# Optimization experiments

Measured on AMD Instinct MI355X. Metric: run time of the kernel, lower is better.

Reference implementation:

```python
import jax, jax.numpy as jnp
import numpy as np
import math

IN_FEATURES = 512
RFF_FEATURES = 2048
OUT_FEATURES = 1000
N = 8192
RIDGE_PENALTY = 1.0
MEAN_FIELD_FACTOR = 25.0
RFF_SCALAR = math.sqrt(RFF_FEATURES / 2)  # 32.0


def _random_ortho(key, n, m):
    q, _ = jnp.linalg.qr(jax.random.normal(key, (n, m), dtype=jnp.float32))
    return q


def setup_inputs() -> dict:
    key = jax.random.key(0)
    k_d, k_w, k_norm, k_b, k_lw, k_lb, k_cov = jax.random.split(key, 7)
    D = jax.random.normal(k_d, (N, IN_FEATURES), dtype=jnp.float32)
    # RFF weight: concat of random orthonormal blocks (rff_features > in_features)
    ws = []
    dim_left = RFF_FEATURES
    kk = k_w
    while dim_left > IN_FEATURES:
        kk, sub = jax.random.split(kk)
        ws.append(_random_ortho(sub, IN_FEATURES, IN_FEATURES))
        dim_left -= IN_FEATURES
    kk, sub = jax.random.split(kk)
    ws.append(_random_ortho(sub, IN_FEATURES, dim_left))
    W = jnp.concatenate(ws, axis=1)  # [in, rff]
    feature_norm = jax.random.normal(k_norm, W.shape, dtype=jnp.float32) ** 2
    W = W * jnp.sqrt(feature_norm.sum(0))
    b = jax.random.uniform(k_b, (RFF_FEATURES,), dtype=jnp.float32) * (2.0 * math.pi)
    # logit head (nn.Linear): weight [out, rff], bias [out]
    bound = 1.0 / math.sqrt(RFF_FEATURES)
    logit_w = jax.random.uniform(k_lw, (OUT_FEATURES, RFF_FEATURES), dtype=jnp.float32,
                                 minval=-bound, maxval=bound)
    logit_b = jax.random.uniform(k_lb, (OUT_FEATURES,), dtype=jnp.float32,
                                 minval=-bound, maxval=bound)
    # positive-definite covariance buffer (stand-in for inverted precision)
    A = jax.random.normal(k_cov, (RFF_FEATURES, RFF_FEATURES), dtype=jnp.float32) * 0.01
    covariance = A @ A.T + jnp.eye(RFF_FEATURES, dtype=jnp.float32)
    return {"D": D, "W": W, "b": b, "logit_w": logit_w, "logit_b": logit_b,
            "covariance": covariance}


def reference(D, W, b, logit_w, logit_b, covariance):
    # RFF feature map: cos(D @ W + b) / rff_scalar  -> [N, rff]
    Phi = jnp.cos(D @ W + b) / RFF_SCALAR
    # linear head -> [N, out]
    pred = Phi @ logit_w.T + logit_b
    # diag(Phi @ cov @ Phi.T) * ridge computed row-wise in O(N*r^2)
    diag_cov = jnp.sum((Phi @ covariance) * Phi, axis=-1) * RIDGE_PENALTY  # [N]
    logits_scale = jnp.sqrt(1.0 + diag_cov * MEAN_FIELD_FACTOR)
    return pred / logits_scale[:, None]
```

## Files before the change

kernel.cpp:

```cpp
#include <hip/hip_runtime.h>
#include <hip/hip_fp8.h>
#include <math.h>

#define N_ROWS 8192
#define IN_F   512
#define RFF    2048
#define OUT_F  1000
#define OUT_PAD 1024
#define INV_RFF_SCALAR 0.03125f
#define MEAN_FIELD 25.0f
#define PHI_NT 24

typedef __attribute__((ext_vector_type(8))) short short8;
typedef __attribute__((ext_vector_type(4))) float f32x4;
typedef __attribute__((ext_vector_type(2))) long long2v;

__device__ __forceinline__ unsigned short f32_to_bf16(float f) {
    unsigned u = __float_as_uint(f);
    unsigned r = 0x7FFFu + ((u >> 16) & 1u);
    return (unsigned short)((u + r) >> 16);
}
__device__ __forceinline__ float bf16_to_f32(unsigned short h) {
    return __uint_as_float(((unsigned)h) << 16);
}
__device__ __forceinline__ unsigned char f32_to_fp8(float x) {
    __hip_fp8_e4m3 q(x);
    return (unsigned char)q.__x;
}

__device__ __forceinline__ int perm64(int k) {
    return (k & ~63) | (((k >> 3) & 3) << 4) | (((k >> 5) & 1) << 3) | (k & 7);
}

__device__ __forceinline__ void stage_tile64(const unsigned short* __restrict__ X,
                                             int r0, int k0, unsigned char* lds,
                                             int w, int lane) {
    #pragma unroll
    for (int h = 0; h < 4; ++h) {
        int qb = h * 256 + w * 64;
        int q = qb + lane;
        int rt = q >> 7, c = (q >> 4) & 7, r = q & 15;
        const void* g = X + (size_t)(r0 + rt * 16 + r) * RFF + k0 + c * 8;
        __builtin_amdgcn_global_load_lds(
            (const __attribute__((address_space(1))) void*)g,
            (__attribute__((address_space(3))) void*)(lds + qb * 16),
            16, 0, 0);
    }
}

__device__ __forceinline__ void stage_tile8(const unsigned char* __restrict__ X,
                                            int r0, int k0b, unsigned char* lds,
                                            int w, int lane) {
    #pragma unroll
    for (int h = 0; h < 4; ++h) {
        int qb = h * 256 + w * 64;
        int q = qb + lane;
        int rt = q >> 7, c = (q >> 4) & 7, r = q & 15;
        const void* g = X + (size_t)(r0 + rt * 16 + r) * RFF + k0b + c * 16;
        __builtin_amdgcn_global_load_lds(
            (const __attribute__((address_space(1))) void*)g,
            (__attribute__((address_space(3))) void*)(lds + qb * 16),
            16, 0, 0);
    }
}

__global__ __launch_bounds__(256) void conv_split_kernel(
    const float* __restrict__ X, unsigned short* __restrict__ H,
    unsigned short* __restrict__ L, int n4)
{
    int i = blockIdx.x * 256 + threadIdx.x;
    if (i >= n4) return;
    float4 v = ((const float4*)X)[i];
    ushort4 h, l;
    h.x = f32_to_bf16(v.x); l.x = f32_to_bf16(v.x - bf16_to_f32(h.x));
    h.y = f32_to_bf16(v.y); l.y = f32_to_bf16(v.y - bf16_to_f32(h.y));
    h.z = f32_to_bf16(v.z); l.z = f32_to_bf16(v.z - bf16_to_f32(h.z));
    h.w = f32_to_bf16(v.w); l.w = f32_to_bf16(v.w - bf16_to_f32(h.w));
    ((ushort4*)H)[i] = h;
    ((ushort4*)L)[i] = l;
}

__global__ __launch_bounds__(256) void conv_covu8_kernel(
    const float* __restrict__ X, unsigned char* __restrict__ O)
{
    int i = blockIdx.x * 256 + threadIdx.x;
    int base = i * 4;
    int row = base >> 11;
    int col = base & 2047;
    int bn = row >> 7, bk = col >> 7;
    float w = (bk < bn) ? 16.0f : (bk == bn ? 8.0f : 0.0f);
    float4 v = ((const float4*)X)[i];
    float w0 = (col + 0 == row) ? 0.0f : w;
    float w1 = (col + 1 == row) ? 0.0f : w;
    float w2 = (col + 2 == row) ? 0.0f : w;
    float w3 = (col + 3 == row) ? 0.0f : w;
    uchar4 o;
    o.x = f32_to_fp8(v.x * w0); o.y = f32_to_fp8(v.y * w1);
    o.z = f32_to_fp8(v.z * w2); o.w = f32_to_fp8(v.w * w3);
    *(uchar4*)(O + (size_t)row * RFF + perm64(col)) = o;
}

__global__ __launch_bounds__(256) void conv_covd_kernel(
    const float* __restrict__ X, float* __restrict__ Cd)
{
    int i = blockIdx.x * 256 + threadIdx.x;
    if (i < RFF) Cd[i] = X[(size_t)i * RFF + i];
}

__global__ __launch_bounds__(256) void conv_phi8_kernel(
    const unsigned short* __restrict__ Phi16, unsigned char* __restrict__ Phi8)
{
    int i = blockIdx.x * 256 + threadIdx.x;
    int base = i * 4;
    int row = base >> 11;
    int col = base & 2047;
    ushort4 v = ((const ushort4*)Phi16)[i];
    uchar4 o;
    o.x = f32_to_fp8(bf16_to_f32(v.x) * 32.0f);
    o.y = f32_to_fp8(bf16_to_f32(v.y) * 32.0f);
    o.z = f32_to_fp8(bf16_to_f32(v.z) * 32.0f);
    o.w = f32_to_fp8(bf16_to_f32(v.w) * 32.0f);
    *(uchar4*)(Phi8 + (size_t)row * RFF + perm64(col)) = o;
}

__global__ __launch_bounds__(256) void conv_lw_kernel(
    const float* __restrict__ Lw, unsigned short* __restrict__ O)
{
    int i = blockIdx.x * 256 + threadIdx.x;
    int base = i * 4;
    int row = base >> 11;
    ushort4 o;
    if (row < OUT_F) {
        float4 v = ((const float4*)Lw)[i];
        o.x = f32_to_bf16(v.x); o.y = f32_to_bf16(v.y);
        o.z = f32_to_bf16(v.z); o.w = f32_to_bf16(v.w);
    } else {
        o.x = o.y = o.z = o.w = 0;
    }
    ((ushort4*)O)[i] = o;
}

__global__ __launch_bounds__(256) void conv_wt_kernel(
    const float* __restrict__ W, unsigned short* __restrict__ TH,
    unsigned short* __restrict__ TL)
{
    __shared__ float tile[64][65];
    const int tid = threadIdx.x;
    const int n0 = blockIdx.x * 64;
    const int k0 = blockIdx.y * 64;
    #pragma unroll
    for (int i = 0; i < 16; ++i) {
        int e = i * 256 + tid;
        int r = e >> 6, c = e & 63;
        tile[r][c] = W[(size_t)(k0 + r) * RFF + n0 + c];
    }
    __syncthreads();
    #pragma unroll
    for (int i = 0; i < 16; ++i) {
        int e = i * 256 + tid;
        int r = e >> 6, c = e & 63;
        float v = tile[c][r];
        unsigned short h = f32_to_bf16(v);
        unsigned short l = f32_to_bf16(v - bf16_to_f32(h));
        TH[(size_t)(n0 + r) * IN_F + k0 + c] = h;
        TL[(size_t)(n0 + r) * IN_F + k0 + c] = l;
    }
}


__device__ __forceinline__ void gload16u(const void* g, unsigned short* lds) {
    __builtin_amdgcn_global_load_lds(
        (const __attribute__((address_space(1))) void*)g,
        (__attribute__((address_space(3))) void*)lds, 16, 0, 0);
}

__device__ __forceinline__ void stageA_g(const unsigned short* __restrict__ src,
                                         int r0, int kk, unsigned short* ldsbuf,
                                         int Qa, int h, int w, int lane) {
    int q   = w * 64 + lane;
    int RTl = h * 8 + Qa * 4 + (q >> 7);
    int c   = (q >> 4) & 7, r = q & 15;
    const void* g = src + (size_t)(r0 + RTl * 16 + r) * IN_F + kk + c * 8;
    int RTu = h * 8 + Qa * 4 + (w >> 1);
    int cu  = (w & 1) * 4;
    gload16u(g, ldsbuf + RTu * 1024 + cu * 128);
}

__device__ __forceinline__ void stageB_g(const unsigned short* __restrict__ src,
                                         int cc0, int kk, unsigned short* ldsbuf,
                                         int nh, int h, int w, int lane) {
    int q    = w * 64 + lane;
    int i    = q >> 7;
    int RTp  = (i >> 1) * 4 + nh * 2 + (i & 1);
    int c    = (q >> 4) & 7, r = q & 15;
    const void* g = src + (size_t)(cc0 + h * 128 + RTp * 16 + r) * IN_F + kk + c * 8;
    int iu   = w >> 1;
    int RTpu = (iu >> 1) * 4 + nh * 2 + (iu & 1);
    int RTu  = h * 8 + RTpu;
    int cu   = (w & 1) * 4;
    gload16u(g, ldsbuf + RTu * 1024 + cu * 128);
}

#define SB0() __builtin_amdgcn_sched_barrier(0)
#define BARRIER() do { SB0(); __builtin_amdgcn_s_barrier(); SB0(); } while (0)
#define WAITVM(N) do { asm volatile("s_waitcnt vmcnt(" #N ")"); SB0(); } while (0)

#define READ_FA(FA, mh) do {                                                  \
    _Pragma("unroll")                                                         \
    for (int i_ = 0; i_ < 4; ++i_) {                                          \
        FA[i_][0] = *(const short8*)(A + (wm * 8 + (mh) * 4 + i_) * 1024      \
                                       + quad * 128 + ln * 8);                \
        FA[i_][1] = *(const short8*)(A + (wm * 8 + (mh) * 4 + i_) * 1024      \
                                       + 512 + quad * 128 + ln * 8);          \
    } } while (0)

#define READ_FB(FB, nh) do {                                                  \
    _Pragma("unroll")                                                         \
    for (int j_ = 0; j_ < 2; ++j_) {                                          \
        FB[j_][0] = *(const short8*)(B + (wn * 4 + (nh) * 2 + j_) * 1024      \
                                       + quad * 128 + ln * 8);                \
        FB[j_][1] = *(const short8*)(B + (wn * 4 + (nh) * 2 + j_) * 1024      \
                                       + 512 + quad * 128 + ln * 8);          \
    } } while (0)

#define MFMA16(MH, NH, FA, FB) do {                                           \
    __builtin_amdgcn_s_setprio(1);                                            \
    _Pragma("unroll")                                                         \
    for (int s_ = 0; s_ < 2; ++s_)                                            \
        _Pragma("unroll")                                                     \
        for (int i_ = 0; i_ < 4; ++i_)                                        \
            _Pragma("unroll")                                                 \
            for (int j_ = 0; j_ < 2; ++j_)                                    \
                acc[(MH) * 4 + i_][(NH) * 2 + j_] =                           \
                    __builtin_amdgcn_mfma_f32_16x16x32_bf16(                  \
                        FA[i_][s_], FB[j_][s_],                               \
                        acc[(MH) * 4 + i_][(NH) * 2 + j_], 0, 0, 0);          \
    __builtin_amdgcn_s_setprio(0);                                            \
} while (0)

__global__ __launch_bounds__(512, 2) void phi_mfma8p_kernel(
    const unsigned short* __restrict__ Dh, const unsigned short* __restrict__ Dl,
    const unsigned short* __restrict__ Wth, const unsigned short* __restrict__ Wtl,
    const float* __restrict__ bias, unsigned short* __restrict__ Phi)
{
    __shared__ unsigned short ldsA[2 * 16384];
    __shared__ unsigned short ldsB[2 * 16384];
    const int tid = threadIdx.x;
    const int w = tid >> 6, lane = tid & 63;
    const int wm = w >> 2, wn = w & 3;
    const int quad = lane >> 4, ln = lane & 15;

    const int bid = blockIdx.x;
    const int xcd = bid & 7, idx = bid >> 3;
    const int rb = (xcd >> 1) * 8 + (idx & 7);
    const int cb = (xcd & 1) * 4 + (idx >> 3);
    const int r0 = rb * 256;
    const int c0 = cb * 256;

    f32x4 acc[8][4];
    #pragma unroll
    for (int i = 0; i < 8; ++i)
        #pragma unroll
        for (int j = 0; j < 4; ++j)
            acc[i][j] = (f32x4)(0.0f);

    stageA_g(Dh,  r0, 0, ldsA, 0, 0, w, lane);
    stageA_g(Dh,  r0, 0, ldsA, 0, 1, w, lane);
    stageA_g(Dh,  r0, 0, ldsA, 1, 0, w, lane);
    stageA_g(Dh,  r0, 0, ldsA, 1, 1, w, lane);
    stageB_g(Wth, c0, 0, ldsB, 0, 0, w, lane);
    stageB_g(Wth, c0, 0, ldsB, 0, 1, w, lane);
    stageB_g(Wth, c0, 0, ldsB, 1, 0, w, lane);
    stageB_g(Wth, c0, 0, ldsB, 1, 1, w, lane);
    stageA_g(Dh,  r0, 64, ldsA + 16384, 0, 0, w, lane);
    stageA_g(Dh,  r0, 64, ldsA + 16384, 0, 1, w, lane);
    stageB_g(Wth, c0, 64, ldsB + 16384, 0, 0, w, lane);
    stageB_g(Wth, c0, 64, ldsB + 16384, 0, 1, w, lane);
    WAITVM(4);
    BARRIER();

    for (int t = 0; t < PHI_NT - 1; ++t) {
        const int buf = t & 1;
        const unsigned short* A = ldsA + buf * 16384;
        const unsigned short* B = ldsB + buf * 16384;
        unsigned short* curA = ldsA + buf * 16384;
        unsigned short* curB = ldsB + buf * 16384;
        unsigned short* othA = ldsA + (buf ^ 1) * 16384;
        unsigned short* othB = ldsB + (buf ^ 1) * 16384;
        const bool has2 = (t + 2) < PHI_NT;
        const int k1 = (t + 1) * 64, k2 = (t + 2) * 64;
        const int kk1 = k1 & 511, kk2 = k2 & 511;
        const unsigned short* A1 = (k1 >= 1024) ? Dl : Dh;
        const unsigned short* B1 = (k1 >= 1024) ? Wth : (k1 >= 512 ? Wtl : Wth);
        const unsigned short* A2 = (k2 >= 1024) ? Dl : Dh;
        const unsigned short* B2 = (k2 >= 1024) ? Wth : (k2 >= 512 ? Wtl : Wth);

        short8 fa[4][2], fb0[2][2], fb1[2][2];

        READ_FA(fa, 0);
        READ_FB(fb0, 0);
        stageA_g(A1, r0, kk1, othA, 1, 0, w, lane);
        stageA_g(A1, r0, kk1, othA, 1, 1, w, lane);
        BARRIER();
        MFMA16(0, 0, fa, fb0);
        BARRIER();

        READ_FB(fb1, 1);
        stageB_g(B1, c0, kk1, othB, 1, 0, w, lane);
        stageB_g(B1, c0, kk1, othB, 1, 1, w, lane);
        BARRIER();
        MFMA16(0, 1, fa, fb1);
        BARRIER();

        READ_FA(fa, 1);
        if (has2) { stageA_g(A2, r0, kk2, curA, 0, 0, w, lane);
                    stageA_g(A2, r0, kk2, curA, 0, 1, w, lane); }
        BARRIER();
        MFMA16(1, 0, fa, fb0);
        BARRIER();

        if (has2) { stageB_g(B2, c0, kk2, curB, 0, 0, w, lane);
                    stageB_g(B2, c0, kk2, curB, 0, 1, w, lane);
                    WAITVM(4); }
        else      { WAITVM(0); }
        BARRIER();
        MFMA16(1, 1, fa, fb1);
        BARRIER();
    }

    {
        asm volatile("" ::: "memory");
        const unsigned short* A = ldsA + ((PHI_NT - 1) & 1) * 16384;
        const unsigned short* B = ldsB + ((PHI_NT - 1) & 1) * 16384;
        short8 fa[4][2], fb0[2][2], fb1[2][2];
        READ_FA(fa, 0);
        READ_FB(fb0, 0);
        READ_FB(fb1, 1);
        MFMA16(0, 0, fa, fb0);
        MFMA16(0, 1, fa, fb1);
        READ_FA(fa, 1);
        MFMA16(1, 0, fa, fb0);
        MFMA16(1, 1, fa, fb1);
    }

    float bv[4];
    #pragma unroll
    for (int nt = 0; nt < 4; ++nt)
        bv[nt] = bias[c0 + wn * 64 + nt * 16 + ln];
    #pragma unroll
    for (int mt = 0; mt < 8; ++mt)
        #pragma unroll
        for (int nt = 0; nt < 4; ++nt) {
            int col = c0 + wn * 64 + nt * 16 + ln;
            #pragma unroll
            for (int reg = 0; reg < 4; ++reg) {
                int row = r0 + wm * 128 + mt * 16 + quad * 4 + reg;
                float z = acc[mt][nt][reg] + bv[nt];
                float p = __cosf(z) * INV_RFF_SCALAR;
                Phi[(size_t)row * RFF + col] = f32_to_bf16(p);
            }
        }
}

__global__ __launch_bounds__(256) void diag8_kernel(
    const unsigned char* __restrict__ Phi8, const unsigned char* __restrict__ CovU8,
    const unsigned short* __restrict__ Phi16, const float* __restrict__ Cd,
    float* __restrict__ diag)
{
    __shared__ __align__(16) unsigned char ldsA[16384];
    __shared__ __align__(16) unsigned char ldsB[16384];
    const int tid = threadIdx.x;
    const int w = tid >> 6, lane = tid & 63;
    const int wm = w >> 1, wn = w & 1;
    const int quad = lane >> 4, ln = lane & 15;
    const int J = 15 - blockIdx.x;
    const int r0 = blockIdx.y * 128;
    const int c0 = J * 128;
    const int kmax = (J + 1) * 128;

    f32x4 acc[4][4];
    #pragma unroll
    for (int i = 0; i < 4; ++i)
        #pragma unroll
        for (int j = 0; j < 4; ++j)
            acc[i][j] = (f32x4)(0.0f);

    for (int k0 = 0; k0 < kmax; k0 += 128) {
        __syncthreads();
        stage_tile8(Phi8,  r0, k0, ldsA, w, lane);
        stage_tile8(CovU8, c0, k0, ldsB, w, lane);
        __syncthreads();

        #pragma unroll
        for (int kb = 0; kb < 2; ++kb) {
            long2v fa[4], fb[4];
            #pragma unroll
            for (int t = 0; t < 4; ++t) {
                fa[t] = *(const long2v*)(ldsA + (((wm * 4 + t) * 128 + (kb * 4 + quad) * 16 + ln) << 4));
                fb[t] = *(const long2v*)(ldsB + (((wn * 4 + t) * 128 + (kb * 4 + quad) * 16 + ln) << 4));
            }
            #pragma unroll
            for (int mt = 0; mt < 4; ++mt)
                #pragma unroll
                for (int nt = 0; nt < 4; ++nt)
                    acc[mt][nt] = __builtin_amdgcn_mfma_f32_16x16x32_fp8_fp8(
                        fa[mt].x, fb[nt].x, acc[mt][nt], 0, 0, 0);
            #pragma unroll
            for (int mt = 0; mt < 4; ++mt)
                #pragma unroll
                for (int nt = 0; nt < 4; ++nt)
                    acc[mt][nt] = __builtin_amdgcn_mfma_f32_16x16x32_fp8_fp8(
                        fa[mt].y, fb[nt].y, acc[mt][nt], 0, 0, 0);
        }
    }

    float cd[4];
    #pragma unroll
    for (int nt = 0; nt < 4; ++nt)
        cd[nt] = 256.0f * Cd[c0 + wn * 64 + nt * 16 + ln];
    #pragma unroll
    for (int mt = 0; mt < 4; ++mt) {
        float psum[4] = {0.f, 0.f, 0.f, 0.f};
        #pragma unroll
        for (int nt = 0; nt < 4; ++nt) {
            int col = c0 + wn * 64 + nt * 16 + ln;
            #pragma unroll
            for (int reg = 0; reg < 4; ++reg) {
                int row = r0 + wm * 64 + mt * 16 + quad * 4 + reg;
                float pv = bf16_to_f32(Phi16[(size_t)row * RFF + col]);
                psum[reg] = fmaf(fmaf(cd[nt], pv, acc[mt][nt][reg]), pv, psum[reg]);
            }
        }
        #pragma unroll
        for (int off = 1; off < 16; off <<= 1)
            #pragma unroll
            for (int reg = 0; reg < 4; ++reg)
                psum[reg] += __shfl_xor(psum[reg], off, 16);
        if (ln == 0) {
            #pragma unroll
            for (int reg = 0; reg < 4; ++reg) {
                int row = r0 + wm * 64 + mt * 16 + quad * 4 + reg;
                atomicAdd(&diag[row], psum[reg] * (1.0f / 256.0f));
            }
        }
    }
}

__global__ __launch_bounds__(256) void pred_mfma_kernel(
    const unsigned short* __restrict__ Phi, const unsigned short* __restrict__ Lw,
    const float* __restrict__ Lb, const float* __restrict__ diag,
    float* __restrict__ out)
{
    __shared__ __align__(16) unsigned char ldsA[16384];
    __shared__ __align__(16) unsigned char ldsB[16384];
    const int tid = threadIdx.x;
    const int w = tid >> 6, lane = tid & 63;
    const int wm = w >> 1, wn = w & 1;
    const int quad = lane >> 4, ln = lane & 15;
    const int r0 = blockIdx.y * 128;
    const int c0 = blockIdx.x * 128;

    f32x4 acc[4][4];
    #pragma unroll
    for (int i = 0; i < 4; ++i)
        #pragma unroll
        for (int j = 0; j < 4; ++j)
            acc[i][j] = (f32x4)(0.0f);

    for (int k0 = 0; k0 < RFF; k0 += 64) {
        __syncthreads();
        stage_tile64(Phi, r0, k0, ldsA, w, lane);
        stage_tile64(Lw,  c0, k0, ldsB, w, lane);
        __syncthreads();

        #pragma unroll
        for (int s = 0; s < 2; ++s) {
            short8 fa[4], fb[4];
            #pragma unroll
            for (int t = 0; t < 4; ++t) {
                fa[t] = *(const short8*)(ldsA + (((wm * 4 + t) * 128 + (s * 4 + quad) * 16 + ln) << 4));
                fb[t] = *(const short8*)(ldsB + (((wn * 4 + t) * 128 + (s * 4 + quad) * 16 + ln) << 4));
            }
            #pragma unroll
            for (int mt = 0; mt < 4; ++mt)
                #pragma unroll
                for (int nt = 0; nt < 4; ++nt)
                    acc[mt][nt] = __builtin_amdgcn_mfma_f32_16x16x32_bf16(
                        fa[mt], fb[nt], acc[mt][nt], 0, 0, 0);
        }
    }

    #pragma unroll
    for (int mt = 0; mt < 4; ++mt) {
        float s[4];
        #pragma unroll
        for (int reg = 0; reg < 4; ++reg) {
            int row = r0 + wm * 64 + mt * 16 + quad * 4 + reg;
            s[reg] = 1.0f / sqrtf(1.0f + MEAN_FIELD * diag[row]);
        }
        #pragma unroll
        for (int nt = 0; nt < 4; ++nt) {
            int col = c0 + wn * 64 + nt * 16 + ln;
            if (col < OUT_F) {
                float bv = Lb[col];
                #pragma unroll
                for (int reg = 0; reg < 4; ++reg) {
                    int row = r0 + wm * 64 + mt * 16 + quad * 4 + reg;
                    out[(size_t)row * OUT_F + col] = (acc[mt][nt][reg] + bv) * s[reg];
                }
            }
        }
    }
}

extern "C" void kernel_launch(void* const* d_in, const int* in_sizes, int n_in,
                              void* d_out, int out_size, void* d_ws, size_t ws_size,
                              hipStream_t stream) {
    const float* D    = (const float*)d_in[0];
    const float* W    = (const float*)d_in[1];
    const float* bias = (const float*)d_in[2];
    const float* Lw   = (const float*)d_in[3];
    const float* Lb   = (const float*)d_in[4];
    const float* cov  = (const float*)d_in[5];
    float* out = (float*)d_out;

    char* p = (char*)d_ws;
    unsigned short* Phi16 = (unsigned short*)p;  p += (size_t)N_ROWS * RFF * 2;
    unsigned char*  Phi8  = (unsigned char*)p;
    unsigned short* Dh    = (unsigned short*)p;  p += (size_t)N_ROWS * IN_F * 2;
    unsigned short* Dl    = (unsigned short*)p;  p += (size_t)N_ROWS * IN_F * 2;
    unsigned short* Wth   = (unsigned short*)p;  p += (size_t)RFF * IN_F * 2;
    unsigned short* Wtl   = (unsigned short*)p;  p += (size_t)RFF * IN_F * 2;
    unsigned short* Lw16  = (unsigned short*)p;  p += (size_t)OUT_PAD * RFF * 2;
    unsigned char*  CovU8 = (unsigned char*)p;
    float*          Cd    = (float*)(p + (size_t)RFF * RFF);
    p += (size_t)RFF * RFF * 2;
    float* diag           = (float*)p;

    hipMemsetAsync(diag, 0, N_ROWS * sizeof(float), stream);

    dim3 blk(256);
    conv_split_kernel<<<dim3((N_ROWS * IN_F / 4 + 255) / 256), blk, 0, stream>>>(D, Dh, Dl, N_ROWS * IN_F / 4);
    conv_wt_kernel<<<dim3(RFF / 64, IN_F / 64), blk, 0, stream>>>(W, Wth, Wtl);
    conv_lw_kernel<<<dim3(OUT_PAD * RFF / 4 / 256), blk, 0, stream>>>(Lw, Lw16);
    conv_covu8_kernel<<<dim3(RFF * RFF / 4 / 256), blk, 0, stream>>>(cov, CovU8);
    conv_covd_kernel<<<dim3(RFF / 256), blk, 0, stream>>>(cov, Cd);

    phi_mfma8p_kernel<<<dim3(256), dim3(512), 0, stream>>>(Dh, Dl, Wth, Wtl, bias, Phi16);
    conv_phi8_kernel<<<dim3(N_ROWS * RFF / 4 / 256), blk, 0, stream>>>(Phi16, Phi8);

    diag8_kernel<<<dim3(16, N_ROWS / 128), blk, 0, stream>>>(Phi8, CovU8, Phi16, Cd, diag);
    pred_mfma_kernel<<<dim3(OUT_PAD / 128, N_ROWS / 128), blk, 0, stream>>>(Phi16, Lw16, Lb, diag, out);
}
```

Baseline: 313.7 us.

## Merge conversion kernels and co-schedule diag and pred GEMMs in one launch

```diff
diff --git a/kernel.cpp b/kernel.cpp
--- a/kernel.cpp
+++ b/kernel.cpp
@@ -30,6 +30,22 @@
 
 __device__ __forceinline__ int perm64(int k) {
     return (k & ~63) | (((k >> 3) & 3) << 4) | (((k >> 5) & 1) << 3) | (k & 7);
+}
+
+__device__ __forceinline__ void stage_tile8(const unsigned char* __restrict__ X,
+                                            int r0, int k0b, unsigned char* lds,
+                                            int w, int lane) {
+    #pragma unroll
+    for (int h = 0; h < 4; ++h) {
+        int qb = h * 256 + w * 64;
+        int q = qb + lane;
+        int rt = q >> 7, c = (q >> 4) & 7, r = q & 15;
+        const void* g = X + (size_t)(r0 + rt * 16 + r) * RFF + k0b + c * 16;
+        __builtin_amdgcn_global_load_lds(
+            (const __attribute__((address_space(1))) void*)g,
+            (__attribute__((address_space(3))) void*)(lds + qb * 16),
+            16, 0, 0);
+    }
 }
 
 __device__ __forceinline__ void stage_tile64(const unsigned short* __restrict__ X,
@@ -48,63 +64,82 @@
     }
 }
 
-__device__ __forceinline__ void stage_tile8(const unsigned char* __restrict__ X,
-                                            int r0, int k0b, unsigned char* lds,
-                                            int w, int lane) {
-    #pragma unroll
-    for (int h = 0; h < 4; ++h) {
-        int qb = h * 256 + w * 64;
-        int q = qb + lane;
-        int rt = q >> 7, c = (q >> 4) & 7, r = q & 15;
-        const void* g = X + (size_t)(r0 + rt * 16 + r) * RFF + k0b + c * 16;
-        __builtin_amdgcn_global_load_lds(
-            (const __attribute__((address_space(1))) void*)g,
-            (__attribute__((address_space(3))) void*)(lds + qb * 16),
-            16, 0, 0);
+__global__ __launch_bounds__(256) void mega_conv_kernel(
+    const float* __restrict__ D, const float* __restrict__ W,
+    const float* __restrict__ Lw, const float* __restrict__ cov,
+    unsigned short* __restrict__ Dh, unsigned short* __restrict__ Dl,
+    unsigned short* __restrict__ Wth, unsigned short* __restrict__ Wtl,
+    unsigned short* __restrict__ Lw16, unsigned char* __restrict__ CovU8,
+    float* __restrict__ Cd)
+{
+    __shared__ float tile[64][65];
+    const int bid = blockIdx.x;
+    const int tid = threadIdx.x;
+
+    if (bid < 4096) {
+        int i = bid * 256 + tid;
+        float4 v = ((const float4*)D)[i];
+        ushort4 h, l;
+        h.x = f32_to_bf16(v.x); l.x = f32_to_bf16(v.x - bf16_to_f32(h.x));
+        h.y = f32_to_bf16(v.y); l.y = f32_to_bf16(v.y - bf16_to_f32(h.y));
+        h.z = f32_to_bf16(v.z); l.z = f32_to_bf16(v.z - bf16_to_f32(h.z));
+        h.w = f32_to_bf16(v.w); l.w = f32_to_bf16(v.w - bf16_to_f32(h.w));
+        ((ushort4*)Dh)[i] = h;
+        ((ushort4*)Dl)[i] = l;
+    } else if (bid < 4352) {
+        int b = bid - 4096;
+        const int n0 = (b & 31) * 64;
+        const int k0 = (b >> 5) * 64;
+        #pragma unroll
+        for (int i = 0; i < 16; ++i) {
+            int e = i * 256 + tid;
+            int r = e >> 6, c = e & 63;
+            tile[r][c] = W[(size_t)(k0 + r) * RFF + n0 + c];
+        }
+        __syncthreads();
+        #pragma unroll
+        for (int i = 0; i < 16; ++i) {
+            int e = i * 256 + tid;
+            int r = e >> 6, c = e & 63;
+            float v = tile[c][r];
+            unsigned short h = f32_to_bf16(v);
+            unsigned short l = f32_to_bf16(v - bf16_to_f32(h));
+            Wth[(size_t)(n0 + r) * IN_F + k0 + c] = h;
+            Wtl[(size_t)(n0 + r) * IN_F + k0 + c] = l;
+        }
+    } else if (bid < 6400) {
+        int i = (bid - 4352) * 256 + tid;
+        int base = i * 4;
+        int row = base >> 11;
+        ushort4 o;
+        if (row < OUT_F) {
+            float4 v = ((const float4*)Lw)[i];
+            o.x = f32_to_bf16(v.x); o.y = f32_to_bf16(v.y);
+            o.z = f32_to_bf16(v.z); o.w = f32_to_bf16(v.w);
+        } else {
+            o.x = o.y = o.z = o.w = 0;
+        }
+        ((ushort4*)Lw16)[i] = o;
+    } else {
+        int i = (bid - 6400) * 256 + tid;
+        int base = i * 4;
+        int row = base >> 11;
+        int col = base & 2047;
+        int bn = row >> 7, bk = col >> 7;
+        float w = (bk < bn) ? 16.0f : (bk == bn ? 8.0f : 0.0f);
+        float4 v = ((const float4*)cov)[i];
+        float vv[4] = {v.x, v.y, v.z, v.w};
+        float wj[4];
+        #pragma unroll
+        for (int j = 0; j < 4; ++j) {
+            if (col + j == row) { wj[j] = 0.0f; Cd[row] = vv[j]; }
+            else wj[j] = w;
+        }
+        uchar4 o;
+        o.x = f32_to_fp8(vv[0] * wj[0]); o.y = f32_to_fp8(vv[1] * wj[1]);
+        o.z = f32_to_fp8(vv[2] * wj[2]); o.w = f32_to_fp8(vv[3] * wj[3]);
+        *(uchar4*)(CovU8 + (size_t)row * RFF + perm64(col)) = o;
     }
-}
-
-__global__ __launch_bounds__(256) void conv_split_kernel(
-    const float* __restrict__ X, unsigned short* __restrict__ H,
-    unsigned short* __restrict__ L, int n4)
-{
-    int i = blockIdx.x * 256 + threadIdx.x;
-    if (i >= n4) return;
-    float4 v = ((const float4*)X)[i];
-    ushort4 h, l;
-    h.x = f32_to_bf16(v.x); l.x = f32_to_bf16(v.x - bf16_to_f32(h.x));
-    h.y = f32_to_bf16(v.y); l.y = f32_to_bf16(v.y - bf16_to_f32(h.y));
-    h.z = f32_to_bf16(v.z); l.z = f32_to_bf16(v.z - bf16_to_f32(h.z));
-    h.w = f32_to_bf16(v.w); l.w = f32_to_bf16(v.w - bf16_to_f32(h.w));
-    ((ushort4*)H)[i] = h;
-    ((ushort4*)L)[i] = l;
-}
-
-__global__ __launch_bounds__(256) void conv_covu8_kernel(
-    const float* __restrict__ X, unsigned char* __restrict__ O)
-{
-    int i = blockIdx.x * 256 + threadIdx.x;
-    int base = i * 4;
-    int row = base >> 11;
-    int col = base & 2047;
-    int bn = row >> 7, bk = col >> 7;
-    float w = (bk < bn) ? 16.0f : (bk == bn ? 8.0f : 0.0f);
-    float4 v = ((const float4*)X)[i];
-    float w0 = (col + 0 == row) ? 0.0f : w;
-    float w1 = (col + 1 == row) ? 0.0f : w;
-    float w2 = (col + 2 == row) ? 0.0f : w;
-    float w3 = (col + 3 == row) ? 0.0f : w;
-    uchar4 o;
-    o.x = f32_to_fp8(v.x * w0); o.y = f32_to_fp8(v.y * w1);
-    o.z = f32_to_fp8(v.z * w2); o.w = f32_to_fp8(v.w * w3);
-    *(uchar4*)(O + (size_t)row * RFF + perm64(col)) = o;
-}
-
-__global__ __launch_bounds__(256) void conv_covd_kernel(
-    const float* __restrict__ X, float* __restrict__ Cd)
-{
-    int i = blockIdx.x * 256 + threadIdx.x;
-    if (i < RFF) Cd[i] = X[(size_t)i * RFF + i];
 }
 
 __global__ __launch_bounds__(256) void conv_phi8_kernel(
@@ -123,50 +158,6 @@
     *(uchar4*)(Phi8 + (size_t)row * RFF + perm64(col)) = o;
 }
 
-__global__ __launch_bounds__(256) void conv_lw_kernel(
-    const float* __restrict__ Lw, unsigned short* __restrict__ O)
-{
-    int i = blockIdx.x * 256 + threadIdx.x;
-    int base = i * 4;
-    int row = base >> 11;
-    ushort4 o;
-    if (row < OUT_F) {
-        float4 v = ((const float4*)Lw)[i];
-        o.x = f32_to_bf16(v.x); o.y = f32_to_bf16(v.y);
-        o.z = f32_to_bf16(v.z); o.w = f32_to_bf16(v.w);
-    } else {
-        o.x = o.y = o.z = o.w = 0;
-    }
-    ((ushort4*)O)[i] = o;
-}
-
-__global__ __launch_bounds__(256) void conv_wt_kernel(
-    const float* __restrict__ W, unsigned short* __restrict__ TH,
-    unsigned short* __restrict__ TL)
-{
-    __shared__ float tile[64][65];
-    const int tid = threadIdx.x;
-    const int n0 = blockIdx.x * 64;
-    const int k0 = blockIdx.y * 64;
-    #pragma unroll
-    for (int i = 0; i < 16; ++i) {
-        int e = i * 256 + tid;
-        int r = e >> 6, c = e & 63;
-        tile[r][c] = W[(size_t)(k0 + r) * RFF + n0 + c];
-    }
-    __syncthreads();
-    #pragma unroll
-    for (int i = 0; i < 16; ++i) {
-        int e = i * 256 + tid;
-        int r = e >> 6, c = e & 63;
-        float v = tile[c][r];
-        unsigned short h = f32_to_bf16(v);
-        unsigned short l = f32_to_bf16(v - bf16_to_f32(h));
-        TH[(size_t)(n0 + r) * IN_F + k0 + c] = h;
-        TL[(size_t)(n0 + r) * IN_F + k0 + c] = l;
-    }
-}
-
 
 __device__ __forceinline__ void gload16u(const void* g, unsigned short* lds) {
     __builtin_amdgcn_global_load_lds(
@@ -174,13 +165,14 @@
         (__attribute__((address_space(3))) void*)lds, 16, 0, 0);
 }
 
-__device__ __forceinline__ void stageA_g(const unsigned short* __restrict__ src,
-                                         int r0, int kk, unsigned short* ldsbuf,
+__device__ __forceinline__ void stage_ab(const unsigned short* __restrict__ src,
+                                         int stride, int r0v, int kk,
+                                         unsigned short* ldsbuf,
                                          int Qa, int h, int w, int lane) {
     int q   = w * 64 + lane;
-    int RTl = h * 8 + Qa * 4 + (q >> 7);
+    int RT  = h * 8 + Qa * 4 + (q >> 7);
     int c   = (q >> 4) & 7, r = q & 15;
-    const void* g = src + (size_t)(r0 + RTl * 16 + r) * IN_F + kk + c * 8;
+    const void* g = src + (size_t)(r0v + RT * 16 + r) * stride + kk + c * 8;
     int RTu = h * 8 + Qa * 4 + (w >> 1);
     int cu  = (w & 1) * 4;
     gload16u(g, ldsbuf + RTu * 1024 + cu * 128);
@@ -204,6 +196,7 @@
 #define SB0() __builtin_amdgcn_sched_barrier(0)
 #define BARRIER() do { SB0(); __builtin_amdgcn_s_barrier(); SB0(); } while (0)
 #define WAITVM(N) do { asm volatile("s_waitcnt vmcnt(" #N ")"); SB0(); } while (0)
+
 
 #define READ_FA(FA, mh) do {                                                  \
     _Pragma("unroll")                                                         \
@@ -264,16 +257,16 @@
         for (int j = 0; j < 4; ++j)
             acc[i][j] = (f32x4)(0.0f);
 
-    stageA_g(Dh,  r0, 0, ldsA, 0, 0, w, lane);
-    stageA_g(Dh,  r0, 0, ldsA, 0, 1, w, lane);
-    stageA_g(Dh,  r0, 0, ldsA, 1, 0, w, lane);
-    stageA_g(Dh,  r0, 0, ldsA, 1, 1, w, lane);
+    stage_ab(Dh, IN_F, r0, 0, ldsA, 0, 0, w, lane);
+    stage_ab(Dh, IN_F, r0, 0, ldsA, 0, 1, w, lane);
+    stage_ab(Dh, IN_F, r0, 0, ldsA, 1, 0, w, lane);
+    stage_ab(Dh, IN_F, r0, 0, ldsA, 1, 1, w, lane);
     stageB_g(Wth, c0, 0, ldsB, 0, 0, w, lane);
     stageB_g(Wth, c0, 0, ldsB, 0, 1, w, lane);
     stageB_g(Wth, c0, 0, ldsB, 1, 0, w, lane);
     stageB_g(Wth, c0, 0, ldsB, 1, 1, w, lane);
-    stageA_g(Dh,  r0, 64, ldsA + 16384, 0, 0, w, lane);
-    stageA_g(Dh,  r0, 64, ldsA + 16384, 0, 1, w, lane);
+    stage_ab(Dh, IN_F, r0, 64, ldsA + 16384, 0, 0, w, lane);
+    stage_ab(Dh, IN_F, r0, 64, ldsA + 16384, 0, 1, w, lane);
     stageB_g(Wth, c0, 64, ldsB + 16384, 0, 0, w, lane);
     stageB_g(Wth, c0, 64, ldsB + 16384, 0, 1, w, lane);
     WAITVM(4);
@@ -299,8 +292,8 @@
 
         READ_FA(fa, 0);
         READ_FB(fb0, 0);
-        stageA_g(A1, r0, kk1, othA, 1, 0, w, lane);
-        stageA_g(A1, r0, kk1, othA, 1, 1, w, lane);
+        stage_ab(A1, IN_F, r0, kk1, othA, 1, 0, w, lane);
+        stage_ab(A1, IN_F, r0, kk1, othA, 1, 1, w, lane);
         BARRIER();
         MFMA16(0, 0, fa, fb0);
         BARRIER();
@@ -313,8 +306,8 @@
         BARRIER();
 
         READ_FA(fa, 1);
-        if (has2) { stageA_g(A2, r0, kk2, curA, 0, 0, w, lane);
-                    stageA_g(A2, r0, kk2, curA, 0, 1, w, lane); }
+        if (has2) { stage_ab(A2, IN_F, r0, kk2, curA, 0, 0, w, lane);
+                    stage_ab(A2, IN_F, r0, kk2, curA, 0, 1, w, lane); }
         BARRIER();
         MFMA16(1, 0, fa, fb0);
         BARRIER();
@@ -362,155 +355,160 @@
         }
 }
 
-__global__ __launch_bounds__(256) void diag8_kernel(
+__global__ __launch_bounds__(256) void fused_dp_kernel(
     const unsigned char* __restrict__ Phi8, const unsigned char* __restrict__ CovU8,
     const unsigned short* __restrict__ Phi16, const float* __restrict__ Cd,
-    float* __restrict__ diag)
+    float* __restrict__ diag, const unsigned short* __restrict__ Lw,
+    float* __restrict__ out)
 {
     __shared__ __align__(16) unsigned char ldsA[16384];
     __shared__ __align__(16) unsigned char ldsB[16384];
+    const int bid = blockIdx.x;
     const int tid = threadIdx.x;
     const int w = tid >> 6, lane = tid & 63;
     const int wm = w >> 1, wn = w & 1;
     const int quad = lane >> 4, ln = lane & 15;
-    const int J = 15 - blockIdx.x;
-    const int r0 = blockIdx.y * 128;
-    const int c0 = J * 128;
-    const int kmax = (J + 1) * 128;
-
-    f32x4 acc[4][4];
-    #pragma unroll
-    for (int i = 0; i < 4; ++i)
-        #pragma unroll
-        for (int j = 0; j < 4; ++j)
-            acc[i][j] = (f32x4)(0.0f);
-
-    for (int k0 = 0; k0 < kmax; k0 += 128) {
-        __syncthreads();
-        stage_tile8(Phi8,  r0, k0, ldsA, w, lane);
-        stage_tile8(CovU8, c0, k0, ldsB, w, lane);
-        __syncthreads();
-
-        #pragma unroll
-        for (int kb = 0; kb < 2; ++kb) {
-            long2v fa[4], fb[4];
-            #pragma unroll
-            for (int t = 0; t < 4; ++t) {
-                fa[t] = *(const long2v*)(ldsA + (((wm * 4 + t) * 128 + (kb * 4 + quad) * 16 + ln) << 4));
-                fb[t] = *(const long2v*)(ldsB + (((wn * 4 + t) * 128 + (kb * 4 + quad) * 16 + ln) << 4));
+    const int m3 = bid % 3;
+
+    if (m3 == 2) {
+        const int pidx = bid / 3;
+        const int r0 = (pidx >> 3) * 128;
+        const int c0 = (pidx & 7) * 128;
+
+        f32x4 acc[4][4];
+        #pragma unroll
+        for (int i = 0; i < 4; ++i)
+            #pragma unroll
+            for (int j = 0; j < 4; ++j)
+                acc[i][j] = (f32x4)(0.0f);
+
+        for (int k0 = 0; k0 < RFF; k0 += 64) {
+            __syncthreads();
+            stage_tile64(Phi16, r0, k0, ldsA, w, lane);
+            stage_tile64(Lw,    c0, k0, ldsB, w, lane);
+            __syncthreads();
+
+            #pragma unroll
+            for (int s = 0; s < 2; ++s) {
+                short8 fa[4], fb[4];
+                #pragma unroll
+                for (int t = 0; t < 4; ++t) {
+                    fa[t] = *(const short8*)(ldsA + (((wm * 4 + t) * 128 + (s * 4 + quad) * 16 + ln) << 4));
+                    fb[t] = *(const short8*)(ldsB + (((wn * 4 + t) * 128 + (s * 4 + quad) * 16 + ln) << 4));
+                }
+                #pragma unroll
+                for (int mt = 0; mt < 4; ++mt)
+                    #pragma unroll
+                    for (int nt = 0; nt < 4; ++nt)
+                        acc[mt][nt] = __builtin_amdgcn_mfma_f32_16x16x32_bf16(
+                            fa[mt], fb[nt], acc[mt][nt], 0, 0, 0);
             }
-            #pragma unroll
-            for (int mt = 0; mt < 4; ++mt)
-                #pragma unroll
-                for (int nt = 0; nt < 4; ++nt)
-                    acc[mt][nt] = __builtin_amdgcn_mfma_f32_16x16x32_fp8_fp8(
-                        fa[mt].x, fb[nt].x, acc[mt][nt], 0, 0, 0);
-            #pragma unroll
-            for (int mt = 0; mt < 4; ++mt)
-                #pragma unroll
-                for (int nt = 0; nt < 4; ++nt)
-                    acc[mt][nt] = __builtin_amdgcn_mfma_f32_16x16x32_fp8_fp8(
-                        fa[mt].y, fb[nt].y, acc[mt][nt], 0, 0, 0);
-        }
-    }
-
-    float cd[4];
-    #pragma unroll
-    for (int nt = 0; nt < 4; ++nt)
-        cd[nt] = 256.0f * Cd[c0 + wn * 64 + nt * 16 + ln];
-    #pragma unroll
-    for (int mt = 0; mt < 4; ++mt) {
-        float psum[4] = {0.f, 0.f, 0.f, 0.f};
-        #pragma unroll
-        for (int nt = 0; nt < 4; ++nt) {
-            int col = c0 + wn * 64 + nt * 16 + ln;
-            #pragma unroll
-            for (int reg = 0; reg < 4; ++reg) {
-                int row = r0 + wm * 64 + mt * 16 + quad * 4 + reg;
-                float pv = bf16_to_f32(Phi16[(size_t)row * RFF + col]);
-                psum[reg] = fmaf(fmaf(cd[nt], pv, acc[mt][nt][reg]), pv, psum[reg]);
+        }
+
+        #pragma unroll
+        for (int mt = 0; mt < 4; ++mt)
+            #pragma unroll
+            for (int nt = 0; nt < 4; ++nt) {
+                int col = c0 + wn * 64 + nt * 16 + ln;
+                if (col < OUT_F) {
+                    #pragma unroll
+                    for (int reg = 0; reg < 4; ++reg) {
+                        int row = r0 + wm * 64 + mt * 16 + quad * 4 + reg;
+                        out[(size_t)row * OUT_F + col] = acc[mt][nt][reg];
+                    }
+                }
             }
-        }
-        #pragma unroll
-        for (int off = 1; off < 16; off <<= 1)
-            #pragma unroll
-            for (int reg = 0; reg < 4; ++reg)
-                psum[reg] += __shfl_xor(psum[reg], off, 16);
-        if (ln == 0) {
-            #pragma unroll
-            for (int reg = 0; reg < 4; ++reg) {
-                int row = r0 + wm * 64 + mt * 16 + quad * 4 + reg;
-                atomicAdd(&diag[row], psum[reg] * (1.0f / 256.0f));
+    } else {
+        const int didx = (bid / 3) * 2 + m3;
+        const int J = 15 - (didx & 15);
+        const int r0 = (didx >> 4) * 128;
+        const int c0 = J * 128;
+        const int kmax = (J + 1) * 128;
+
+        f32x4 acc[4][4];
+        #pragma unroll
+        for (int i = 0; i < 4; ++i)
+            #pragma unroll
+            for (int j = 0; j < 4; ++j)
+                acc[i][j] = (f32x4)(0.0f);
+
+        for (int k0 = 0; k0 < kmax; k0 += 128) {
+            __syncthreads();
+            stage_tile8(Phi8,  r0, k0, ldsA, w, lane);
+            stage_tile8(CovU8, c0, k0, ldsB, w, lane);
+            __syncthreads();
+
+            #pragma unroll
+            for (int kb = 0; kb < 2; ++kb) {
+                long2v fa[4], fb[4];
+                #pragma unroll
+                for (int t = 0; t < 4; ++t) {
+                    fa[t] = *(const long2v*)(ldsA + (((wm * 4 + t) * 128 + (kb * 4 + quad) * 16 + ln) << 4));
+                    fb[t] = *(const long2v*)(ldsB + (((wn * 4 + t) * 128 + (kb * 4 + quad) * 16 + ln) << 4));
+                }
+                #pragma unroll
+                for (int mt = 0; mt < 4; ++mt)
+                    #pragma unroll
+                    for (int nt = 0; nt < 4; ++nt)
+                        acc[mt][nt] = __builtin_amdgcn_mfma_f32_16x16x32_fp8_fp8(
+                            fa[mt].x, fb[nt].x, acc[mt][nt], 0, 0, 0);
+                #pragma unroll
+                for (int mt = 0; mt < 4; ++mt)
+                    #pragma unroll
+                    for (int nt = 0; nt < 4; ++nt)
+                        acc[mt][nt] = __builtin_amdgcn_mfma_f32_16x16x32_fp8_fp8(
+                            fa[mt].y, fb[nt].y, acc[mt][nt], 0, 0, 0);
             }
         }
-    }
-}
-
-__global__ __launch_bounds__(256) void pred_mfma_kernel(
-    const unsigned short* __restrict__ Phi, const unsigned short* __restrict__ Lw,
-    const float* __restrict__ Lb, const float* __restrict__ diag,
-    float* __restrict__ out)
-{
-    __shared__ __align__(16) unsigned char ldsA[16384];
-    __shared__ __align__(16) unsigned char ldsB[16384];
-    const int tid = threadIdx.x;
-    const int w = tid >> 6, lane = tid & 63;
-    const int wm = w >> 1, wn = w & 1;
-    const int quad = lane >> 4, ln = lane & 15;
-    const int r0 = blockIdx.y * 128;
-    const int c0 = blockIdx.x * 128;
-
-    f32x4 acc[4][4];
-    #pragma unroll
-    for (int i = 0; i < 4; ++i)
-        #pragma unroll
-        for (int j = 0; j < 4; ++j)
-            acc[i][j] = (f32x4)(0.0f);
-
-    for (int k0 = 0; k0 < RFF; k0 += 64) {
-        __syncthreads();
-        stage_tile64(Phi, r0, k0, ldsA, w, lane);
-        stage_tile64(Lw,  c0, k0, ldsB, w, lane);
-        __syncthreads();
-
-        #pragma unroll
-        for (int s = 0; s < 2; ++s) {
-            short8 fa[4], fb[4];
-            #pragma unroll
-            for (int t = 0; t < 4; ++t) {
-                fa[t] = *(const short8*)(ldsA + (((wm * 4 + t) * 128 + (s * 4 + quad) * 16 + ln) << 4));
-                fb[t] = *(const short8*)(ldsB + (((wn * 4 + t) * 128 + (s * 4 + quad) * 16 + ln) << 4));
-            }
-            #pragma unroll
-            for (int mt = 0; mt < 4; ++mt)
-                #pragma unroll
-                for (int nt = 0; nt < 4; ++nt)
-                    acc[mt][nt] = __builtin_amdgcn_mfma_f32_16x16x32_bf16(
-                        fa[mt], fb[nt], acc[mt][nt], 0, 0, 0);
-        }
-    }
-
-    #pragma unroll
-    for (int mt = 0; mt < 4; ++mt) {
-        float s[4];
-        #pragma unroll
-        for (int reg = 0; reg < 4; ++reg) {
-            int row = r0 + wm * 64 + mt * 16 + quad * 4 + reg;
-            s[reg] = 1.0f / sqrtf(1.0f + MEAN_FIELD * diag[row]);
-        }
-        #pragma unroll
-        for (int nt = 0; nt < 4; ++nt) {
-            int col = c0 + wn * 64 + nt * 16 + ln;
-            if (col < OUT_F) {
-                float bv = Lb[col];
+
+        float cd[4];
+        #pragma unroll
+        for (int nt = 0; nt < 4; ++nt)
+            cd[nt] = 256.0f * Cd[c0 + wn * 64 + nt * 16 + ln];
+        #pragma unroll
+        for (int mt = 0; mt < 4; ++mt) {
+            float psum[4] = {0.f, 0.f, 0.f, 0.f};
+            #pragma unroll
+            for (int nt = 0; nt < 4; ++nt) {
+                int col = c0 + wn * 64 + nt * 16 + ln;
                 #pragma unroll
                 for (int reg = 0; reg < 4; ++reg) {
                     int row = r0 + wm * 64 + mt * 16 + quad * 4 + reg;
-                    out[(size_t)row * OUT_F + col] = (acc[mt][nt][reg] + bv) * s[reg];
+                    float pv = bf16_to_f32(Phi16[(size_t)row * RFF + col]);
+                    psum[reg] = fmaf(fmaf(cd[nt], pv, acc[mt][nt][reg]), pv, psum[reg]);
                 }
             }
+            #pragma unroll
+            for (int off = 1; off < 16; off <<= 1)
+                #pragma unroll
+                for (int reg = 0; reg < 4; ++reg)
+                    psum[reg] += __shfl_xor(psum[reg], off, 16);
+            if (ln == 0) {
+                #pragma unroll
+                for (int reg = 0; reg < 4; ++reg) {
+                    int row = r0 + wm * 64 + mt * 16 + quad * 4 + reg;
+                    atomicAdd(&diag[row], psum[reg] * (1.0f / 256.0f));
+                }
+            }
         }
     }
+}
+
+__global__ __launch_bounds__(256) void pred_epilogue_kernel(
+    float* __restrict__ out, const float* __restrict__ Lb,
+    const float* __restrict__ diag)
+{
+    int i = blockIdx.x * 256 + threadIdx.x;
+    int row = i / 250;
+    int c = (i - row * 250) * 4;
+    float s = 1.0f / sqrtf(1.0f + MEAN_FIELD * diag[row]);
+    float4 v = *(float4*)(out + (size_t)row * OUT_F + c);
+    float4 b = *(const float4*)(Lb + c);
+    v.x = (v.x + b.x) * s;
+    v.y = (v.y + b.y) * s;
+    v.z = (v.z + b.z) * s;
+    v.w = (v.w + b.w) * s;
+    *(float4*)(out + (size_t)row * OUT_F + c) = v;
 }
 
 extern "C" void kernel_launch(void* const* d_in, const int* in_sizes, int n_in,
@@ -539,16 +537,14 @@
 
     hipMemsetAsync(diag, 0, N_ROWS * sizeof(float), stream);
 
-    dim3 blk(256);
-    conv_split_kernel<<<dim3((N_ROWS * IN_F / 4 + 255) / 256), blk, 0, stream>>>(D, Dh, Dl, N_ROWS * IN_F / 4);
-    conv_wt_kernel<<<dim3(RFF / 64, IN_F / 64), blk, 0, stream>>>(W, Wth, Wtl);
-    conv_lw_kernel<<<dim3(OUT_PAD * RFF / 4 / 256), blk, 0, stream>>>(Lw, Lw16);
-    conv_covu8_kernel<<<dim3(RFF * RFF / 4 / 256), blk, 0, stream>>>(cov, CovU8);
-    conv_covd_kernel<<<dim3(RFF / 256), blk, 0, stream>>>(cov, Cd);
+    mega_conv_kernel<<<dim3(10496), dim3(256), 0, stream>>>(
+        D, W, Lw, cov, Dh, Dl, Wth, Wtl, Lw16, CovU8, Cd);
 
     phi_mfma8p_kernel<<<dim3(256), dim3(512), 0, stream>>>(Dh, Dl, Wth, Wtl, bias, Phi16);
-    conv_phi8_kernel<<<dim3(N_ROWS * RFF / 4 / 256), blk, 0, stream>>>(Phi16, Phi8);
-
-    diag8_kernel<<<dim3(16, N_ROWS / 128), blk, 0, stream>>>(Phi8, CovU8, Phi16, Cd, diag);
-    pred_mfma_kernel<<<dim3(OUT_PAD / 128, N_ROWS / 128), blk, 0, stream>>>(Phi16, Lw16, Lb, diag, out);
-}
+    conv_phi8_kernel<<<dim3(N_ROWS * RFF / 4 / 256), dim3(256), 0, stream>>>(Phi16, Phi8);
+
+    fused_dp_kernel<<<dim3(1536), dim3(256), 0, stream>>>(
+        Phi8, CovU8, Phi16, Cd, diag, Lw16, out);
+
+    pred_epilogue_kernel<<<dim3(N_ROWS * 250 / 256), dim3(256), 0, stream>>>(out, Lb, diag);
+}
```

Result: slower. 327.1 us (+4.3%).
